# Kernel optimization log

Hardware: AMD Instinct MI355X
Metric: run time of the kernel (lower is better)

## Reference

```python
import jax, jax.numpy as jnp
import numpy as np

N_NODES = 50000
N_EDGES = 800000
N_GRAPHS = 64
IN_CH = 128
EMB = 64


def gcn_conv(x, W, b, src, dst, w, n):
    """PyG GCNConv: add self-loops (weight 1), symmetric normalization,
    linear transform, scatter-sum aggregation, bias."""
    loop = jnp.arange(n, dtype=src.dtype)
    src2 = jnp.concatenate([src, loop])
    dst2 = jnp.concatenate([dst, loop])
    w2 = jnp.concatenate([w, jnp.ones((n,), dtype=x.dtype)])
    deg = jax.ops.segment_sum(w2, dst2, num_segments=n)
    dinv = jnp.where(deg > 0, jax.lax.rsqrt(jnp.where(deg > 0, deg, 1.0)), 0.0)
    norm = dinv[src2] * w2 * dinv[dst2]  # [E+N]
    h = x @ W  # [N, out]
    msg = norm[:, None] * h[src2]  # [E+N, out]
    return jax.ops.segment_sum(msg, dst2, num_segments=n) + b


def setup_inputs() -> dict:
    key = jax.random.key(0)
    ks = jax.random.split(key, 16)
    x = jax.random.normal(ks[0], (N_NODES, IN_CH), dtype=jnp.float32)
    edge_index = jax.random.randint(ks[1], (2, N_EDGES), 0, N_NODES, dtype=jnp.int32)
    edge_attr = jax.random.uniform(ks[2], (N_EDGES,), dtype=jnp.float32)
    batch_index = jnp.sort(jax.random.randint(ks[3], (N_NODES,), 0, N_GRAPHS, dtype=jnp.int32))
    def glorot(k, shape):
        lim = float(np.sqrt(6.0 / (shape[0] + shape[1])))
        return jax.random.uniform(k, shape, dtype=jnp.float32, minval=-lim, maxval=lim)
    return {
        "x": x, "edge_index": edge_index, "edge_attr": edge_attr, "batch_index": batch_index,
        "W0": glorot(ks[4], (IN_CH, EMB)), "b0": jnp.zeros((EMB,), jnp.float32),
        "W1": glorot(ks[5], (EMB, EMB)), "b1": jnp.zeros((EMB,), jnp.float32),
        "W2": glorot(ks[6], (EMB, EMB)), "b2": jnp.zeros((EMB,), jnp.float32),
        "W3": glorot(ks[7], (EMB, EMB)), "b3": jnp.zeros((EMB,), jnp.float32),
        "Wout": glorot(ks[8], (2 * EMB, 1)), "bout": jnp.zeros((1,), jnp.float32),
    }


def reference(x, edge_index, edge_attr, batch_index, W0, b0, W1, b1, W2, b2, W3, b3, Wout, bout):
    n = x.shape[0]
    src, dst = edge_index[0], edge_index[1]
    h = jnp.tanh(gcn_conv(x, W0, b0, src, dst, edge_attr, n))
    h = jnp.tanh(gcn_conv(h, W1, b1, src, dst, edge_attr, n))
    h = jnp.tanh(gcn_conv(h, W2, b2, src, dst, edge_attr, n))
    h = jnp.tanh(gcn_conv(h, W3, b3, src, dst, edge_attr, n))
    gmax = jax.ops.segment_max(h, batch_index, num_segments=N_GRAPHS)
    gsum = jax.ops.segment_sum(h, batch_index, num_segments=N_GRAPHS)
    cnt = jax.ops.segment_sum(jnp.ones((n,), h.dtype), batch_index, num_segments=N_GRAPHS)
    gmean = gsum / jnp.maximum(cnt, 1.0)[:, None]
    pooled = jnp.concatenate([gmax, gmean], axis=1)  # [B, 2*EMB]
    return (pooled @ Wout + bout).reshape(-1)
```

## Files before the change

### kernel.cpp

```cpp
#include <hip/hip_runtime.h>
#include <hip/hip_fp16.h>
#include <math.h>
#include <limits.h>

#define N_NODES 50000
#define N_EDGES 800000
#define N_GRAPHS 64
#define IN_CH 128
#define EMB 64
#define POOL_CHUNK 16
#define CPAD64 16
#define CNT_SHIFT 44
#define FX_SCALE 16777216.0f

typedef _Float16 f16;
typedef __attribute__((ext_vector_type(8))) _Float16 half8;
typedef __attribute__((ext_vector_type(4))) float f32x4;

__global__ void init_k(unsigned long long* cnt64, int* total, int* gmax,
                       float* gsum, int* cnt) {
    int i = blockIdx.x * blockDim.x + threadIdx.x;
    if (i < N_NODES * CPAD64) cnt64[i] = 0ULL;
    if (i == 0) *total = 0;
    if (i < N_GRAPHS * EMB) { gmax[i] = INT_MIN; gsum[i] = 0.f; }
    if (i < N_GRAPHS) cnt[i] = 0;
}

__global__ void hist_k(const int* __restrict__ dst, const float* __restrict__ w,
                       unsigned long long* cnt64, int* __restrict__ slot_in) {
    int e = blockIdx.x * blockDim.x + threadIdx.x;
    if (e >= N_EDGES) return;
    unsigned long long fx = (unsigned long long)(w[e] * FX_SCALE + 0.5f);
    unsigned long long old = atomicAdd(&cnt64[(size_t)dst[e] * CPAD64],
                                       (1ULL << CNT_SHIFT) | fx);
    slot_in[e] = (int)(old >> CNT_SHIFT);
}

__global__ void alloc_k(const unsigned long long* __restrict__ cnt64,
                        int* __restrict__ row_start, int* __restrict__ row_end,
                        int* total, float* __restrict__ dinv) {
    int i = blockIdx.x * blockDim.x + threadIdx.x;
    int lane = threadIdx.x & 63;
    unsigned long long v = (i < N_NODES) ? cnt64[(size_t)i * CPAD64] : 0ULL;
    int c = (int)(v >> CNT_SHIFT);
    int inc = c;
    for (int off = 1; off < 64; off <<= 1) {
        int t = __shfl_up(inc, off);
        if (lane >= off) inc += t;
    }
    int base;
    if (lane == 63) base = atomicAdd(total, inc);
    base = __shfl(base, 63);
    int excl = base + inc - c;
    if (i < N_NODES) {
        row_start[i] = excl;
        row_end[i] = excl + c;
        float degw = (float)(v & ((1ULL << CNT_SHIFT) - 1)) * (1.0f / FX_SCALE);
        float d = 1.0f + degw;
        dinv[i] = d > 0.f ? rsqrtf(d) : 0.f;
    }
}

__global__ void scatter_k(const int* __restrict__ src, const int* __restrict__ dst,
                          const float* __restrict__ w, const int* __restrict__ slot_in,
                          const int* __restrict__ row_start, int2* __restrict__ csr) {
    int e = blockIdx.x * blockDim.x + threadIdx.x;
    if (e >= N_EDGES) return;
    int d = dst[e];
    int slot = row_start[d] + slot_in[e];
    csr[slot] = make_int2(src[e] * (EMB * 2), __float_as_int(w[e]));
}

template<int K, bool HALF_IN>
__global__ __launch_bounds__(256) void gemm_k(const void* __restrict__ A_,
                                              const float* __restrict__ W,
                                              const float* __restrict__ dinv,
                                              __half* __restrict__ out) {
    constexpr int LDK = K + 8;
    __shared__ __align__(16) f16 Al[64 * LDK];
    __shared__ __align__(16) f16 Wt[EMB * LDK];
    int tid = threadIdx.x;
    long rowBase = (long)blockIdx.x * 64;
    int validRows = (int)min((long)64, (long)N_NODES - rowBase);

    if constexpr (HALF_IN) {
        const __half* Ah = (const __half*)A_ + rowBase * K;
        constexpr int CH = K / 8;
        for (int i = tid; i < validRows * CH; i += 256) {
            int r = i / CH, c = i % CH;
            uint4 v = *(const uint4*)(Ah + (long)r * K + c * 8);
            *(uint4*)&Al[r * LDK + c * 8] = v;
        }
    } else {
        const float* Af = (const float*)A_;
        constexpr int CH = K / 4;
        for (int i = tid; i < validRows * CH; i += 256) {
            int r = i / CH, c = i % CH;
            float4 v = *(const float4*)(Af + (rowBase + r) * K + c * 4);
            __half2 p0 = __floats2half2_rn(v.x, v.y);
            __half2 p1 = __floats2half2_rn(v.z, v.w);
            uint2 u = make_uint2(*(unsigned int*)&p0, *(unsigned int*)&p1);
            *(uint2*)&Al[r * LDK + c * 4] = u;
        }
    }
    {
        constexpr int CZ = K / 8;
        for (int i = tid + validRows * CZ; i < 64 * CZ; i += 256) {
            int r = i / CZ, c = i % CZ;
            *(uint4*)&Al[r * LDK + c * 8] = make_uint4(0, 0, 0, 0);
        }
    }
    {
        const float4* Wg = (const float4*)W;
        for (int i = tid; i < K * (EMB / 4); i += 256) {
            int k = i >> 4, nq = i & 15;
            float4 v = Wg[i];
            Wt[(4 * nq + 0) * LDK + k] = (f16)v.x;
            Wt[(4 * nq + 1) * LDK + k] = (f16)v.y;
            Wt[(4 * nq + 2) * LDK + k] = (f16)v.z;
            Wt[(4 * nq + 3) * LDK + k] = (f16)v.w;
        }
    }
    __syncthreads();

    int wv = tid >> 6, lane = tid & 63;
    int l15 = lane & 15, kg = (lane >> 4) * 8;
    const f16* Ap = &Al[(wv * 16 + l15) * LDK + kg];
    const f16* Bp = &Wt[l15 * LDK + kg];
    f32x4 acc0 = {0.f, 0.f, 0.f, 0.f};
    f32x4 acc1 = acc0, acc2 = acc0, acc3 = acc0;
#pragma unroll
    for (int ks = 0; ks < K / 32; ++ks) {
        int k0 = ks * 32;
        half8 a  = *(const half8*)(Ap + k0);
        half8 b0 = *(const half8*)(Bp + k0);
        half8 b1 = *(const half8*)(Bp + 16 * LDK + k0);
        half8 b2 = *(const half8*)(Bp + 32 * LDK + k0);
        half8 b3 = *(const half8*)(Bp + 48 * LDK + k0);
        acc0 = __builtin_amdgcn_mfma_f32_16x16x32_f16(a, b0, acc0, 0, 0, 0);
        acc1 = __builtin_amdgcn_mfma_f32_16x16x32_f16(a, b1, acc1, 0, 0, 0);
        acc2 = __builtin_amdgcn_mfma_f32_16x16x32_f16(a, b2, acc2, 0, 0, 0);
        acc3 = __builtin_amdgcn_mfma_f32_16x16x32_f16(a, b3, acc3, 0, 0, 0);
    }
    int orow = wv * 16 + (lane >> 4) * 4;
#pragma unroll
    for (int i = 0; i < 4; ++i) {
        long row = rowBase + orow + i;
        if (row >= N_NODES) break;
        float dv = dinv[row];
        __half* op = &out[row * EMB + l15];
        op[0]  = __float2half(dv * acc0[i]);
        op[16] = __float2half(dv * acc1[i]);
        op[32] = __float2half(dv * acc2[i]);
        op[48] = __float2half(dv * acc3[i]);
    }
}

__global__ __launch_bounds__(256) void fused_agg_k(const __half* __restrict__ hs,
                                                   const int2* __restrict__ csr,
                                                   const int* __restrict__ row_start,
                                                   const int* __restrict__ row_end,
                                                   const float* __restrict__ dinv,
                                                   const float* __restrict__ b,
                                                   __half* __restrict__ out) {
    int node = (blockIdx.x * blockDim.x + threadIdx.x) >> 6;
    int lane = threadIdx.x & 63;
    if (node >= N_NODES) return;
    const char* hsb = (const char*)hs + (size_t)(lane * 2);
    float di = dinv[node];
    float acc = __half2float(hs[(long)node * EMB + lane]);
    int e = row_start[node];
    int end = row_end[node];
    for (; e + 7 < end; e += 8) {
        int2 rl = csr[e + (lane & 7)];
        int so[8], wb[8];
#pragma unroll
        for (int i = 0; i < 8; ++i) {
            so[i] = __builtin_amdgcn_readlane(rl.x, i);
            wb[i] = __builtin_amdgcn_readlane(rl.y, i);
        }
        __half v[8];
#pragma unroll
        for (int i = 0; i < 8; ++i) v[i] = *(const __half*)(hsb + (unsigned)so[i]);
#pragma unroll
        for (int i = 0; i < 8; ++i) acc += __int_as_float(wb[i]) * __half2float(v[i]);
    }
    for (; e + 3 < end; e += 4) {
        int2 r0 = csr[e], r1 = csr[e + 1], r2 = csr[e + 2], r3 = csr[e + 3];
        float v0 = __half2float(*(const __half*)(hsb + (unsigned)r0.x));
        float v1 = __half2float(*(const __half*)(hsb + (unsigned)r1.x));
        float v2 = __half2float(*(const __half*)(hsb + (unsigned)r2.x));
        float v3 = __half2float(*(const __half*)(hsb + (unsigned)r3.x));
        acc += __int_as_float(r0.y) * v0;
        acc += __int_as_float(r1.y) * v1;
        acc += __int_as_float(r2.y) * v2;
        acc += __int_as_float(r3.y) * v3;
    }
    for (; e < end; ++e) {
        int2 r0 = csr[e];
        acc += __int_as_float(r0.y) * __half2float(*(const __half*)(hsb + (unsigned)r0.x));
    }
    float o = tanhf(di * acc + b[lane]);
    __half oh = __float2half(o);
    __builtin_nontemporal_store(*(unsigned short*)&oh,
                                (unsigned short*)&out[(long)node * EMB + lane]);
}

__device__ inline int f2ord(float x) {
    int bb = __float_as_int(x);
    return bb >= 0 ? bb : (bb ^ 0x7fffffff);
}
__device__ inline float ord2f(int k) {
    return __int_as_float(k >= 0 ? k : (k ^ 0x7fffffff));
}

__global__ __launch_bounds__(256) void pool_k(const __half* __restrict__ h,
                                              const int* __restrict__ batch,
                                              int* gmax, float* gsum, int* cnt) {
    int wave = (blockIdx.x * blockDim.x + threadIdx.x) >> 6;
    int lane = threadIdx.x & 63;
    int start = wave * POOL_CHUNK;
    if (start >= N_NODES) return;
    int bsel = (lane < POOL_CHUNK) ? batch[start + lane] : 0;
    float v[POOL_CHUNK];
#pragma unroll
    for (int i = 0; i < POOL_CHUNK; ++i)
        v[i] = __half2float(h[(long)(start + i) * EMB + lane]);
    int curg = __shfl(bsel, 0);
    float mx = -INFINITY, sm = 0.f;
    int ct = 0;
#pragma unroll
    for (int i = 0; i < POOL_CHUNK; ++i) {
        int g = __shfl(bsel, i);
        if (g != curg) {
            atomicMax(&gmax[curg * EMB + lane], f2ord(mx));
            atomicAdd(&gsum[curg * EMB + lane], sm);
            if (lane == 0) atomicAdd(&cnt[curg], ct);
            curg = g; mx = -INFINITY; sm = 0.f; ct = 0;
        }
        mx = fmaxf(mx, v[i]);
        sm += v[i];
        ++ct;
    }
    atomicMax(&gmax[curg * EMB + lane], f2ord(mx));
    atomicAdd(&gsum[curg * EMB + lane], sm);
    if (lane == 0) atomicAdd(&cnt[curg], ct);
}

__global__ void final_k(const int* __restrict__ gmax, const float* __restrict__ gsum,
                        const int* __restrict__ cnt, const float* __restrict__ Wout,
                        const float* __restrict__ bout, float* __restrict__ out) {
    int g = threadIdx.x;
    if (g >= N_GRAPHS) return;
    float c = fmaxf((float)cnt[g], 1.0f);
    float acc = bout[0];
    for (int ch = 0; ch < EMB; ++ch) {
        acc += ord2f(gmax[g * EMB + ch]) * Wout[ch]
             + (gsum[g * EMB + ch] / c) * Wout[EMB + ch];
    }
    out[g] = acc;
}

extern "C" void kernel_launch(void* const* d_in, const int* in_sizes, int n_in,
                              void* d_out, int out_size, void* d_ws, size_t ws_size,
                              hipStream_t stream) {
    const float* x         = (const float*)d_in[0];
    const int*   edge_idx  = (const int*)d_in[1];
    const float* edge_attr = (const float*)d_in[2];
    const int*   batch     = (const int*)d_in[3];
    const float* W0 = (const float*)d_in[4];
    const float* b0 = (const float*)d_in[5];
    const float* W1 = (const float*)d_in[6];
    const float* b1 = (const float*)d_in[7];
    const float* W2 = (const float*)d_in[8];
    const float* b2 = (const float*)d_in[9];
    const float* W3 = (const float*)d_in[10];
    const float* b3 = (const float*)d_in[11];
    const float* Wout = (const float*)d_in[12];
    const float* bout = (const float*)d_in[13];
    float* out = (float*)d_out;

    const int* src = edge_idx;
    const int* dst = edge_idx + N_EDGES;

    char* ws = (char*)d_ws;
    float*  dinv      = (float*)ws;  ws += (size_t)N_NODES * sizeof(float);
    unsigned long long* cnt64 = (unsigned long long*)ws;
    ws += (size_t)N_NODES * CPAD64 * sizeof(unsigned long long);
    int*    row_start = (int*)ws;    ws += (size_t)N_NODES * sizeof(int);
    int*    row_end   = (int*)ws;    ws += (size_t)N_NODES * sizeof(int);
    int*    slot_in   = (int*)ws;    ws += (size_t)N_EDGES * sizeof(int);
    int*    total     = (int*)ws;    ws += 4 * sizeof(int);
    int2*   csr       = (int2*)ws;   ws += (size_t)N_EDGES * sizeof(int2);
    __half* bufL      = (__half*)ws; ws += (size_t)N_NODES * EMB * sizeof(__half);
    __half* bufH      = (__half*)ws; ws += (size_t)N_NODES * EMB * sizeof(__half);
    int*    gmax      = (int*)ws;    ws += N_GRAPHS * EMB * sizeof(int);
    float*  gsum      = (float*)ws;  ws += N_GRAPHS * EMB * sizeof(float);
    int*    cnt       = (int*)ws;    ws += N_GRAPHS * sizeof(int);

    const int nodeB = (N_NODES + 255) / 256;
    const int edgeB = (N_EDGES + 255) / 256;
    const int waveB = (N_NODES * 64 + 255) / 256;
    const int gemmB = (N_NODES + 63) / 64;
    const int initB = (N_NODES * CPAD64 + 255) / 256;

    init_k<<<initB, 256, 0, stream>>>(cnt64, total, gmax, gsum, cnt);
    hist_k<<<edgeB, 256, 0, stream>>>(dst, edge_attr, cnt64, slot_in);
    alloc_k<<<nodeB, 256, 0, stream>>>(cnt64, row_start, row_end, total, dinv);
    scatter_k<<<edgeB, 256, 0, stream>>>(src, dst, edge_attr, slot_in, row_start, csr);

    const float* Wl[4] = {W0, W1, W2, W3};
    const float* bl[4] = {b0, b1, b2, b3};
    for (int l = 0; l < 4; ++l) {
        if (l == 0) gemm_k<IN_CH, false><<<gemmB, 256, 0, stream>>>(x, Wl[0], dinv, bufL);
        else        gemm_k<EMB, true>   <<<gemmB, 256, 0, stream>>>(bufH, Wl[l], dinv, bufL);
        fused_agg_k<<<waveB, 256, 0, stream>>>(bufL, csr, row_start, row_end, dinv, bl[l], bufH);
    }

    pool_k<<<(((N_NODES + POOL_CHUNK - 1) / POOL_CHUNK) * 64 + 255) / 256, 256, 0, stream>>>(
        bufH, batch, gmax, gsum, cnt);
    final_k<<<1, 64, 0, stream>>>(gmax, gsum, cnt, Wout, bout, out);
}
```

Before: 343.0 us.

## Fuse aggregation with next layer GEMM and final aggregation with pooling

Replaces the per-layer aggregate-then-GEMM kernel pairs with a single kernel that aggregates 64 nodes into shared memory, applies tanh, then runs the next layer's MFMA GEMM directly from LDS. The last aggregation is fused with the graph pooling so the final hidden state never goes to global memory. The edge tail loop is also rewritten to use lane-broadcast loads. This removes intermediate half-precision round trips through global memory and several launches, at the cost of 512-thread blocks with 8 nodes per wave, which may reduce latency hiding for the irregular gather.

```diff
diff --git a/kernel.cpp b/kernel.cpp
--- a/kernel.cpp
+++ b/kernel.cpp
@@ -71,6 +71,39 @@
     csr[slot] = make_int2(src[e] * (EMB * 2), __float_as_int(w[e]));
 }
 
+__device__ inline float agg_row(const char* hsb, const int2* __restrict__ csr,
+                                int e, int end, float acc) {
+    for (; e + 7 < end; e += 8) {
+        int2 rl = csr[e + (threadIdx.x & 7)];
+        int so[8], wb[8];
+#pragma unroll
+        for (int j = 0; j < 8; ++j) {
+            so[j] = __builtin_amdgcn_readlane(rl.x, j);
+            wb[j] = __builtin_amdgcn_readlane(rl.y, j);
+        }
+        __half v[8];
+#pragma unroll
+        for (int j = 0; j < 8; ++j) v[j] = *(const __half*)(hsb + (unsigned)so[j]);
+#pragma unroll
+        for (int j = 0; j < 8; ++j) acc += __int_as_float(wb[j]) * __half2float(v[j]);
+    }
+    int n = end - e;
+    if (n > 0) {
+        int idx = e + (threadIdx.x & 7);
+        if (idx >= end) idx = end - 1;
+        int2 rl = csr[idx];
+#pragma unroll
+        for (int j = 0; j < 8; ++j) {
+            if (j < n) {
+                int so = __builtin_amdgcn_readlane(rl.x, j);
+                int wb = __builtin_amdgcn_readlane(rl.y, j);
+                acc += __int_as_float(wb) * __half2float(*(const __half*)(hsb + (unsigned)so));
+            }
+        }
+    }
+    return acc;
+}
+
 template<int K, bool HALF_IN>
 __global__ __launch_bounds__(256) void gemm_k(const void* __restrict__ A_,
                                               const float* __restrict__ W,
@@ -156,54 +189,82 @@
     }
 }
 
-__global__ __launch_bounds__(256) void fused_agg_k(const __half* __restrict__ hs,
-                                                   const int2* __restrict__ csr,
-                                                   const int* __restrict__ row_start,
-                                                   const int* __restrict__ row_end,
-                                                   const float* __restrict__ dinv,
-                                                   const float* __restrict__ b,
-                                                   __half* __restrict__ out) {
-    int node = (blockIdx.x * blockDim.x + threadIdx.x) >> 6;
-    int lane = threadIdx.x & 63;
-    if (node >= N_NODES) return;
-    const char* hsb = (const char*)hs + (size_t)(lane * 2);
-    float di = dinv[node];
-    float acc = __half2float(hs[(long)node * EMB + lane]);
-    int e = row_start[node];
-    int end = row_end[node];
-    for (; e + 7 < end; e += 8) {
-        int2 rl = csr[e + (lane & 7)];
-        int so[8], wb[8];
-#pragma unroll
+__global__ __launch_bounds__(512) void agg_gemm_k(const __half* __restrict__ hs_in,
+                                                  const int2* __restrict__ csr,
+                                                  const int* __restrict__ row_start,
+                                                  const int* __restrict__ row_end,
+                                                  const float* __restrict__ dinv,
+                                                  const float* __restrict__ b,
+                                                  const float* __restrict__ W,
+                                                  __half* __restrict__ hs_out) {
+    constexpr int K = EMB;
+    constexpr int LDK = K + 8;
+    __shared__ __align__(16) f16 Ao[64 * LDK];
+    __shared__ __align__(16) f16 Wt[EMB * LDK];
+    int tid = threadIdx.x;
+    int wv = tid >> 6, lane = tid & 63;
+    long tileBase = (long)blockIdx.x * 64;
+    int validRows = (int)min((long)64, (long)N_NODES - tileBase);
+
+    {
+        const float4* Wg = (const float4*)W;
+        for (int i = tid; i < K * (EMB / 4); i += 512) {
+            int k = i >> 4, nq = i & 15;
+            float4 v = Wg[i];
+            Wt[(4 * nq + 0) * LDK + k] = (f16)v.x;
+            Wt[(4 * nq + 1) * LDK + k] = (f16)v.y;
+            Wt[(4 * nq + 2) * LDK + k] = (f16)v.z;
+            Wt[(4 * nq + 3) * LDK + k] = (f16)v.w;
+        }
+    }
+    {
+        const char* hsb = (const char*)hs_in + (size_t)(lane * 2);
+        float bl = b[lane];
         for (int i = 0; i < 8; ++i) {
-            so[i] = __builtin_amdgcn_readlane(rl.x, i);
-            wb[i] = __builtin_amdgcn_readlane(rl.y, i);
-        }
-        __half v[8];
-#pragma unroll
-        for (int i = 0; i < 8; ++i) v[i] = *(const __half*)(hsb + (unsigned)so[i]);
-#pragma unroll
-        for (int i = 0; i < 8; ++i) acc += __int_as_float(wb[i]) * __half2float(v[i]);
-    }
-    for (; e + 3 < end; e += 4) {
-        int2 r0 = csr[e], r1 = csr[e + 1], r2 = csr[e + 2], r3 = csr[e + 3];
-        float v0 = __half2float(*(const __half*)(hsb + (unsigned)r0.x));
-        float v1 = __half2float(*(const __half*)(hsb + (unsigned)r1.x));
-        float v2 = __half2float(*(const __half*)(hsb + (unsigned)r2.x));
-        float v3 = __half2float(*(const __half*)(hsb + (unsigned)r3.x));
-        acc += __int_as_float(r0.y) * v0;
-        acc += __int_as_float(r1.y) * v1;
-        acc += __int_as_float(r2.y) * v2;
-        acc += __int_as_float(r3.y) * v3;
-    }
-    for (; e < end; ++e) {
-        int2 r0 = csr[e];
-        acc += __int_as_float(r0.y) * __half2float(*(const __half*)(hsb + (unsigned)r0.x));
-    }
-    float o = tanhf(di * acc + b[lane]);
-    __half oh = __float2half(o);
-    __builtin_nontemporal_store(*(unsigned short*)&oh,
-                                (unsigned short*)&out[(long)node * EMB + lane]);
+            long node = tileBase + wv * 8 + i;
+            if (node >= N_NODES) break;
+            float di = dinv[node];
+            float acc = __half2float(hs_in[node * EMB + lane]);
+            acc = agg_row(hsb, csr, row_start[node], row_end[node], acc);
+            float o = tanhf(di * acc + bl);
+            Ao[(wv * 8 + i) * LDK + lane] = (f16)o;
+        }
+    }
+    if (validRows < 64) {
+        for (int i = tid; i < (64 - validRows) * (K / 8); i += 512) {
+            int r = validRows + i / (K / 8), c = i % (K / 8);
+            *(uint4*)&Ao[r * LDK + c * 8] = make_uint4(0, 0, 0, 0);
+        }
+    }
+    __syncthreads();
+    {
+        int l15 = lane & 15, kg = (lane >> 4) * 8;
+        int r0 = (wv & 3) * 16;
+        int ch = (wv >> 2) * 32;
+        const f16* Ap  = &Ao[(r0 + l15) * LDK + kg];
+        const f16* Bp0 = &Wt[(ch + l15) * LDK + kg];
+        const f16* Bp1 = &Wt[(ch + 16 + l15) * LDK + kg];
+        f32x4 acc0 = {0.f, 0.f, 0.f, 0.f}, acc1 = acc0;
+#pragma unroll
+        for (int ks = 0; ks < K / 32; ++ks) {
+            int k0 = ks * 32;
+            half8 a  = *(const half8*)(Ap + k0);
+            half8 b0 = *(const half8*)(Bp0 + k0);
+            half8 b1 = *(const half8*)(Bp1 + k0);
+            acc0 = __builtin_amdgcn_mfma_f32_16x16x32_f16(a, b0, acc0, 0, 0, 0);
+            acc1 = __builtin_amdgcn_mfma_f32_16x16x32_f16(a, b1, acc1, 0, 0, 0);
+        }
+        int orow = r0 + (lane >> 4) * 4;
+#pragma unroll
+        for (int i = 0; i < 4; ++i) {
+            long row = tileBase + orow + i;
+            if (row >= N_NODES) break;
+            float dv = dinv[row];
+            __half* op = &hs_out[row * EMB + ch + l15];
+            op[0]  = __float2half(dv * acc0[i]);
+            op[16] = __float2half(dv * acc1[i]);
+        }
+    }
 }
 
 __device__ inline int f2ord(float x) {
@@ -214,37 +275,60 @@
     return __int_as_float(k >= 0 ? k : (k ^ 0x7fffffff));
 }
 
-__global__ __launch_bounds__(256) void pool_k(const __half* __restrict__ h,
-                                              const int* __restrict__ batch,
-                                              int* gmax, float* gsum, int* cnt) {
-    int wave = (blockIdx.x * blockDim.x + threadIdx.x) >> 6;
-    int lane = threadIdx.x & 63;
-    int start = wave * POOL_CHUNK;
-    if (start >= N_NODES) return;
-    int bsel = (lane < POOL_CHUNK) ? batch[start + lane] : 0;
-    float v[POOL_CHUNK];
-#pragma unroll
-    for (int i = 0; i < POOL_CHUNK; ++i)
-        v[i] = __half2float(h[(long)(start + i) * EMB + lane]);
-    int curg = __shfl(bsel, 0);
-    float mx = -INFINITY, sm = 0.f;
-    int ct = 0;
-#pragma unroll
-    for (int i = 0; i < POOL_CHUNK; ++i) {
-        int g = __shfl(bsel, i);
-        if (g != curg) {
-            atomicMax(&gmax[curg * EMB + lane], f2ord(mx));
-            atomicAdd(&gsum[curg * EMB + lane], sm);
-            if (lane == 0) atomicAdd(&cnt[curg], ct);
-            curg = g; mx = -INFINITY; sm = 0.f; ct = 0;
-        }
-        mx = fmaxf(mx, v[i]);
-        sm += v[i];
-        ++ct;
-    }
-    atomicMax(&gmax[curg * EMB + lane], f2ord(mx));
-    atomicAdd(&gsum[curg * EMB + lane], sm);
-    if (lane == 0) atomicAdd(&cnt[curg], ct);
+__global__ __launch_bounds__(512) void agg_pool_k(const __half* __restrict__ hs_in,
+                                                  const int2* __restrict__ csr,
+                                                  const int* __restrict__ row_start,
+                                                  const int* __restrict__ row_end,
+                                                  const float* __restrict__ dinv,
+                                                  const float* __restrict__ b,
+                                                  const int* __restrict__ batch,
+                                                  int* gmax, float* gsum, int* cnt) {
+    __shared__ float Ho[64 * EMB];
+    int tid = threadIdx.x;
+    int wv = tid >> 6, lane = tid & 63;
+    long tileBase = (long)blockIdx.x * 64;
+
+    {
+        const char* hsb = (const char*)hs_in + (size_t)(lane * 2);
+        float bl = b[lane];
+        for (int i = 0; i < 8; ++i) {
+            long node = tileBase + wv * 8 + i;
+            if (node >= N_NODES) break;
+            float di = dinv[node];
+            float acc = __half2float(hs_in[node * EMB + lane]);
+            acc = agg_row(hsb, csr, row_start[node], row_end[node], acc);
+            Ho[(wv * 8 + i) * EMB + lane] = tanhf(di * acc + bl);
+        }
+    }
+    __syncthreads();
+    if (wv < 4) {
+        long start = tileBase + wv * POOL_CHUNK;
+        if (start >= N_NODES) return;
+        int bsel = (lane < POOL_CHUNK) ? batch[start + lane] : 0;
+        float v[POOL_CHUNK];
+#pragma unroll
+        for (int i = 0; i < POOL_CHUNK; ++i)
+            v[i] = Ho[(wv * 16 + i) * EMB + lane];
+        int curg = __shfl(bsel, 0);
+        float mx = -INFINITY, sm = 0.f;
+        int ct = 0;
+#pragma unroll
+        for (int i = 0; i < POOL_CHUNK; ++i) {
+            int g = __shfl(bsel, i);
+            if (g != curg) {
+                atomicMax(&gmax[curg * EMB + lane], f2ord(mx));
+                atomicAdd(&gsum[curg * EMB + lane], sm);
+                if (lane == 0) atomicAdd(&cnt[curg], ct);
+                curg = g; mx = -INFINITY; sm = 0.f; ct = 0;
+            }
+            mx = fmaxf(mx, v[i]);
+            sm += v[i];
+            ++ct;
+        }
+        atomicMax(&gmax[curg * EMB + lane], f2ord(mx));
+        atomicAdd(&gsum[curg * EMB + lane], sm);
+        if (lane == 0) atomicAdd(&cnt[curg], ct);
+    }
 }
 
 __global__ void final_k(const int* __restrict__ gmax, const float* __restrict__ gsum,
@@ -293,14 +377,13 @@
     int*    total     = (int*)ws;    ws += 4 * sizeof(int);
     int2*   csr       = (int2*)ws;   ws += (size_t)N_EDGES * sizeof(int2);
     __half* bufL      = (__half*)ws; ws += (size_t)N_NODES * EMB * sizeof(__half);
-    __half* bufH      = (__half*)ws; ws += (size_t)N_NODES * EMB * sizeof(__half);
+    __half* bufM      = (__half*)ws; ws += (size_t)N_NODES * EMB * sizeof(__half);
     int*    gmax      = (int*)ws;    ws += N_GRAPHS * EMB * sizeof(int);
     float*  gsum      = (float*)ws;  ws += N_GRAPHS * EMB * sizeof(float);
     int*    cnt       = (int*)ws;    ws += N_GRAPHS * sizeof(int);
 
     const int nodeB = (N_NODES + 255) / 256;
     const int edgeB = (N_EDGES + 255) / 256;
-    const int waveB = (N_NODES * 64 + 255) / 256;
     const int gemmB = (N_NODES + 63) / 64;
     const int initB = (N_NODES * CPAD64 + 255) / 256;
 
@@ -309,15 +392,11 @@
     alloc_k<<<nodeB, 256, 0, stream>>>(cnt64, row_start, row_end, total, dinv);
     scatter_k<<<edgeB, 256, 0, stream>>>(src, dst, edge_attr, slot_in, row_start, csr);
 
-    const float* Wl[4] = {W0, W1, W2, W3};
-    const float* bl[4] = {b0, b1, b2, b3};
-    for (int l = 0; l < 4; ++l) {
-        if (l == 0) gemm_k<IN_CH, false><<<gemmB, 256, 0, stream>>>(x, Wl[0], dinv, bufL);
-        else        gemm_k<EMB, true>   <<<gemmB, 256, 0, stream>>>(bufH, Wl[l], dinv, bufL);
-        fused_agg_k<<<waveB, 256, 0, stream>>>(bufL, csr, row_start, row_end, dinv, bl[l], bufH);
-    }
-
-    pool_k<<<(((N_NODES + POOL_CHUNK - 1) / POOL_CHUNK) * 64 + 255) / 256, 256, 0, stream>>>(
-        bufH, batch, gmax, gsum, cnt);
+    gemm_k<IN_CH, false><<<gemmB, 256, 0, stream>>>(x, W0, dinv, bufL);
+    agg_gemm_k<<<gemmB, 512, 0, stream>>>(bufL, csr, row_start, row_end, dinv, b0, W1, bufM);
+    agg_gemm_k<<<gemmB, 512, 0, stream>>>(bufM, csr, row_start, row_end, dinv, b1, W2, bufL);
+    agg_gemm_k<<<gemmB, 512, 0, stream>>>(bufL, csr, row_start, row_end, dinv, b2, W3, bufM);
+    agg_pool_k<<<gemmB, 512, 0, stream>>>(bufM, csr, row_start, row_end, dinv, b3,
+                                          batch, gmax, gsum, cnt);
     final_k<<<1, 64, 0, stream>>>(gmax, gsum, cnt, Wout, bout, out);
 }
```

New measurement: 319.3 us. 1.07x faster.
